# Optimization experiments

Hardware: AMD Instinct MI355X
Metric: run time of the kernel (lower is better)

The kernel has to match this reference:

```python
import jax, jax.numpy as jnp
import numpy as np

D_MODEL = 2048
N_HEADS = 16
N_KV = 4
HEAD_DIM = D_MODEL // N_HEADS  # 128
KV_DIM = N_KV * HEAD_DIM       # 512
CLIP = 8.0
EPS = 1e-5
THETA = 500000.0


def setup_inputs() -> dict:
    key = jax.random.key(0)
    ks = jax.random.split(key, 12)
    B, T = 2, 2048
    std = 0.02
    return {
        "x": jax.random.normal(ks[0], (B, T, D_MODEL), jnp.float32),
        "wq": jax.random.normal(ks[1], (D_MODEL, D_MODEL), jnp.float32) * std,
        "bq": jnp.zeros((D_MODEL,), jnp.float32),
        "wk": jax.random.normal(ks[2], (KV_DIM, D_MODEL), jnp.float32) * std,
        "bk": jnp.zeros((KV_DIM,), jnp.float32),
        "wv": jax.random.normal(ks[3], (KV_DIM, D_MODEL), jnp.float32) * std,
        "bv": jnp.zeros((KV_DIM,), jnp.float32),
        "wo": jax.random.normal(ks[4], (D_MODEL, D_MODEL), jnp.float32) * std,
        "bo": jnp.zeros((D_MODEL,), jnp.float32),
        "q_gamma": jnp.ones((D_MODEL,), jnp.float32),
        "q_beta": jnp.zeros((D_MODEL,), jnp.float32),
        "k_gamma": jnp.ones((KV_DIM,), jnp.float32),
        "k_beta": jnp.zeros((KV_DIM,), jnp.float32),
    }


def _layernorm(x, gamma, beta):
    mu = jnp.mean(x, axis=-1, keepdims=True)
    var = jnp.mean(jnp.square(x - mu), axis=-1, keepdims=True)
    return (x - mu) * jax.lax.rsqrt(var + EPS) * gamma + beta


def _rope(q, k):
    # q: (B,T,H,Dh), k: (B,T,Hkv,Dh); non-interleaved rotate-half RoPE
    T = q.shape[1]
    half = HEAD_DIM // 2
    inv_freq = 1.0 / (THETA ** (jnp.arange(0, half, dtype=jnp.float32) * 2.0 / HEAD_DIM))
    freqs = jnp.arange(T, dtype=jnp.float32)[:, None] * inv_freq[None, :]  # (T, half)
    emb = jnp.concatenate([freqs, freqs], axis=-1)  # (T, Dh)
    cos = jnp.cos(emb)[None, :, None, :]
    sin = jnp.sin(emb)[None, :, None, :]

    def rot_half(x):
        x1, x2 = x[..., :half], x[..., half:]
        return jnp.concatenate([-x2, x1], axis=-1)

    q = q * cos + rot_half(q) * sin
    k = k * cos + rot_half(k) * sin
    return q, k


def reference(x, wq, bq, wk, bk, wv, bv, wo, bo, q_gamma, q_beta, k_gamma, k_beta):
    B, T, _ = x.shape
    q = x @ wq.T + bq            # (B,T,D)
    k = x @ wk.T + bk            # (B,T,KV_DIM)
    v = x @ wv.T + bv
    q = jnp.clip(q, -CLIP, CLIP)
    k = jnp.clip(k, -CLIP, CLIP)
    v = jnp.clip(v, -CLIP, CLIP)
    q = _layernorm(q, q_gamma, q_beta)
    k = _layernorm(k, k_gamma, k_beta)
    q = q.reshape(B, T, N_HEADS, HEAD_DIM)
    k = k.reshape(B, T, N_KV, HEAD_DIM)
    v = v.reshape(B, T, N_KV, HEAD_DIM)
    q, k = _rope(q, k)
    # to (B,H,T,Dh)
    q = q.transpose(0, 2, 1, 3)
    k = k.transpose(0, 2, 1, 3)
    v = v.transpose(0, 2, 1, 3)
    g = N_HEADS // N_KV
    # GQA repeat_interleave via broadcast: (B,Hkv,T,Dh) -> (B,H,T,Dh)
    k = jnp.broadcast_to(k[:, :, None], (B, N_KV, g, T, HEAD_DIM)).reshape(B, N_HEADS, T, HEAD_DIM)
    v = jnp.broadcast_to(v[:, :, None], (B, N_KV, g, T, HEAD_DIM)).reshape(B, N_HEADS, T, HEAD_DIM)
    scale = 1.0 / jnp.sqrt(jnp.float32(HEAD_DIM))
    scores = jnp.einsum('bhqd,bhkd->bhqk', q, k) * scale
    causal = jnp.tril(jnp.ones((T, T), dtype=bool))
    scores = jnp.where(causal[None, None], scores, jnp.finfo(scores.dtype).min)
    att = jax.nn.softmax(scores, axis=-1)
    out = jnp.einsum('bhqk,bhkd->bhqd', att, v)     # (B,H,T,Dh)
    out = out.transpose(0, 2, 1, 3).reshape(B, T, D_MODEL)
    return out @ wo.T + bo
```

## Files before the change

### kernel.cpp

```cpp
#include <hip/hip_runtime.h>
#include <hip/hip_bf16.h>
#include <math.h>

typedef __bf16 bf16;
typedef __attribute__((ext_vector_type(8))) bf16 bf16x8;
typedef __attribute__((ext_vector_type(2))) bf16 bf16x2;
typedef __attribute__((ext_vector_type(4))) float f32x4;

#define LOG2E 1.4426950408889634f
#define LOG2_THETA 18.931568569324174f

#if __has_builtin(__builtin_amdgcn_exp2f)
#define EXP2F __builtin_amdgcn_exp2f
#else
#define EXP2F exp2f
#endif

__device__ inline void async_cp16(const void* gptr, void* lptr) {
  __builtin_amdgcn_global_load_lds(
      (const __attribute__((address_space(1))) unsigned int*)gptr,
      (__attribute__((address_space(3))) unsigned int*)lptr, 16, 0, 0);
}

__global__ __launch_bounds__(256) void cast_all(
    const float* __restrict__ x,  const float* __restrict__ wq,
    const float* __restrict__ wk, const float* __restrict__ wv,
    const float* __restrict__ wo, bf16* __restrict__ xb,
    bf16* __restrict__ wqkvb, bf16* __restrict__ wob) {
  const int bx = blockIdx.x;
  const size_t gi = ((size_t)bx * 256 + threadIdx.x) * 8;
  const float* src;
  bf16* dst;
  if (bx < 4096)      { src = x  + gi;              dst = xb + gi; }
  else if (bx < 6144) { src = wq + (gi -  8388608); dst = wqkvb + (gi - 8388608); }
  else if (bx < 6656) { src = wk + (gi - 12582912); dst = wqkvb + 4194304 + (gi - 12582912); }
  else if (bx < 7168) { src = wv + (gi - 13631488); dst = wqkvb + 5242880 + (gi - 13631488); }
  else                { src = wo + (gi - 14680064); dst = wob + (gi - 14680064); }
  float4 a = *(const float4*)(src);
  float4 b = *(const float4*)(src + 4);
  bf16x8 o;
  o[0] = (bf16)a.x; o[1] = (bf16)a.y; o[2] = (bf16)a.z; o[3] = (bf16)a.w;
  o[4] = (bf16)b.x; o[5] = (bf16)b.y; o[6] = (bf16)b.z; o[7] = (bf16)b.w;
  *(bf16x8*)dst = o;
}

template <typename OUT_T, bool QKV, bool CLIP>
__global__ __launch_bounds__(256) void gemm_bt(
    const bf16* __restrict__ A, const bf16* __restrict__ W,
    const float* __restrict__ b0, const float* __restrict__ b1,
    const float* __restrict__ b2, OUT_T* __restrict__ C,
    int M, int N, int K) {
  __shared__ bf16 As[2][128 * 32];
  __shared__ bf16 Bs[2][128 * 32];
  const int nwg = gridDim.x * gridDim.y;
  int lid = blockIdx.x + gridDim.x * blockIdx.y;
  lid = (lid & 7) * (nwg >> 3) + (lid >> 3);
  const int m0 = (lid & 31) * 128, n0 = (lid >> 5) * 128;
  const int t = threadIdx.x;
  const int w = t >> 6, lane = t & 63, quad = lane >> 4, l15 = lane & 15;
  const int wm = (w >> 1) * 64, wn = (w & 1) * 64;

  f32x4 acc[4][4];
#pragma unroll
  for (int i = 0; i < 4; i++)
#pragma unroll
    for (int j = 0; j < 4; j++) acc[i][j] = (f32x4)0.0f;

  int soff[2], ldso[2];
#pragma unroll
  for (int i = 0; i < 2; i++) {
    const int c = w * 128 + i * 64 + lane;
    const int r = c >> 2;
    const int sl = (c & 3) ^ (r & 3);
    soff[i] = r * K + sl * 8;
    ldso[i] = (w * 128 + i * 64) * 16;
  }
  const bf16* Abase = A + (size_t)m0 * K;
  const bf16* Wbase = W + (size_t)n0 * K;

  const int fseg = (quad ^ (l15 & 3)) * 8;

#pragma unroll
  for (int i = 0; i < 2; i++) {
    async_cp16(Abase + soff[i], (char*)&As[0][0] + ldso[i]);
    async_cp16(Wbase + soff[i], (char*)&Bs[0][0] + ldso[i]);
  }
  __asm__ volatile("s_waitcnt vmcnt(0)" ::: "memory");
  __builtin_amdgcn_s_barrier();
  __builtin_amdgcn_sched_barrier(0);

  int cur = 0;
  for (int k0 = 0; k0 < K; k0 += 32) {
    if (k0 + 32 < K) {
      const int nxt = cur ^ 1;
#pragma unroll
      for (int i = 0; i < 2; i++) {
        async_cp16(Abase + k0 + 32 + soff[i], (char*)&As[nxt][0] + ldso[i]);
        async_cp16(Wbase + k0 + 32 + soff[i], (char*)&Bs[nxt][0] + ldso[i]);
      }
    }
    __builtin_amdgcn_sched_barrier(0);

    bf16x8 af[4], bfr[4];
#pragma unroll
    for (int i = 0; i < 4; i++)
      af[i] = *(const bf16x8*)(&As[cur][0] + (wm + i * 16 + l15) * 32 + fseg);
#pragma unroll
    for (int j = 0; j < 4; j++)
      bfr[j] = *(const bf16x8*)(&Bs[cur][0] + (wn + j * 16 + l15) * 32 + fseg);
#pragma unroll
    for (int i = 0; i < 4; i++)
#pragma unroll
      for (int j = 0; j < 4; j++)
        acc[i][j] = __builtin_amdgcn_mfma_f32_16x16x32_bf16(af[i], bfr[j], acc[i][j], 0, 0, 0);

    __asm__ volatile("s_waitcnt vmcnt(0)" ::: "memory");
    __builtin_amdgcn_s_barrier();
    __builtin_amdgcn_sched_barrier(0);
    cur ^= 1;
  }

#pragma unroll
  for (int i = 0; i < 4; i++)
#pragma unroll
    for (int j = 0; j < 4; j++) {
      const int col = n0 + wn + j * 16 + l15;
      float bval;
      if (QKV) {
        if (col < 2048) bval = b0[col];
        else if (col < 2560) bval = b1[col - 2048];
        else bval = b2[col - 2560];
      } else {
        bval = b0[col];
      }
#pragma unroll
      for (int r = 0; r < 4; r++) {
        const int row = m0 + wm + i * 16 + quad * 4 + r;
        float v = acc[i][j][r] + bval;
        if (CLIP) v = fminf(fmaxf(v, -8.0f), 8.0f);
        C[(size_t)row * N + col] = (OUT_T)v;
      }
    }
}

__global__ __launch_bounds__(256) void fused_mid(
    const bf16* __restrict__ X, const float* __restrict__ qg,
    const float* __restrict__ qb, const float* __restrict__ kg,
    const float* __restrict__ kb, bf16* __restrict__ Qr,
    bf16* __restrict__ Kr, bf16* __restrict__ Vt) {
  __shared__ bf16 smt[64][136];
  __shared__ float red[8];
  __shared__ float tcs[64], tsn[64];
  __shared__ float ktab_c[4][64], ktab_s[4][64];
  const int bx = blockIdx.x;
  const int tid = threadIdx.x;
  const int w = tid >> 6, lane = tid & 63;

  if (bx < 4096) {
    const int row = bx, b = row >> 11, tpos = row & 2047;
    if (tid < 64) {
      const float inv = exp2f((float)tid * (-LOG2_THETA / 64.0f));
      float sn, cs;
      sincosf((float)tpos * inv, &sn, &cs);
      tcs[tid] = cs; tsn[tid] = sn;
    }
    const bf16* x = X + (size_t)row * 3072;
    bf16x8 xi = *(const bf16x8*)(x + tid * 8);
    float v[8];
    float s = 0.0f;
#pragma unroll
    for (int e = 0; e < 8; e++) { v[e] = (float)xi[e]; s += v[e]; }
#pragma unroll
    for (int m = 32; m >= 1; m >>= 1) s += __shfl_xor(s, m, 64);
    if (lane == 0) red[w] = s;
    __syncthreads();
    const float mean = (red[0] + red[1] + red[2] + red[3]) * (1.0f / 2048.0f);
    float vs = 0.0f;
#pragma unroll
    for (int e = 0; e < 8; e++) { float d = v[e] - mean; vs += d * d; }
#pragma unroll
    for (int m = 32; m >= 1; m >>= 1) vs += __shfl_xor(vs, m, 64);
    if (lane == 0) red[4 + w] = vs;
    __syncthreads();
    const float var = (red[4] + red[5] + red[6] + red[7]) * (1.0f / 2048.0f);
    const float rstd = rsqrtf(var + 1e-5f);
    const int c0 = tid * 8;
    const float4 g0 = *(const float4*)(qg + c0);
    const float4 g1 = *(const float4*)(qg + c0 + 4);
    const float4 b0v = *(const float4*)(qb + c0);
    const float4 b1v = *(const float4*)(qb + c0 + 4);
    const float gA[8] = {g0.x, g0.y, g0.z, g0.w, g1.x, g1.y, g1.z, g1.w};
    const float bA[8] = {b0v.x, b0v.y, b0v.z, b0v.w, b1v.x, b1v.y, b1v.z, b1v.w};
    float y[8];
#pragma unroll
    for (int e = 0; e < 8; e++) y[e] = (v[e] - mean) * rstd * gA[e] + bA[e];
    const int h = c0 >> 7;
    bf16x8 ov;
#pragma unroll
    for (int e = 0; e < 8; e++) {
      const int c = c0 + e, d = c & 127, i = d & 63;
      const float part = __shfl_xor(y[e], 8, 64);
      const float rot = (d < 64) ? -part : part;
      ov[e] = (bf16)(y[e] * tcs[i] + rot * tsn[i]);
    }
    *(bf16x8*)(Qr + ((size_t)(b * 16 + h) * 2048 + tpos) * 128 + (c0 & 127)) = ov;
  } else if (bx < 5120) {
    const int idx = bx - 4096;
    const int row = idx * 4 + w, b = row >> 11, tpos = row & 2047;
    {
      const float inv = exp2f((float)lane * (-LOG2_THETA / 64.0f));
      float sn, cs;
      sincosf((float)tpos * inv, &sn, &cs);
      ktab_c[w][lane] = cs; ktab_s[w][lane] = sn;
    }
    __syncthreads();
    const bf16* x = X + (size_t)row * 3072 + 2048;
    bf16x8 xi = *(const bf16x8*)(x + lane * 8);
    float v[8];
    float s = 0.0f;
#pragma unroll
    for (int e = 0; e < 8; e++) { v[e] = (float)xi[e]; s += v[e]; }
#pragma unroll
    for (int m = 32; m >= 1; m >>= 1) s += __shfl_xor(s, m, 64);
    const float mean = s * (1.0f / 512.0f);
    float vs = 0.0f;
#pragma unroll
    for (int e = 0; e < 8; e++) { float d = v[e] - mean; vs += d * d; }
#pragma unroll
    for (int m = 32; m >= 1; m >>= 1) vs += __shfl_xor(vs, m, 64);
    const float var = vs * (1.0f / 512.0f);
    const float rstd = rsqrtf(var + 1e-5f);
    const int c0 = lane * 8;
    const float4 g0 = *(const float4*)(kg + c0);
    const float4 g1 = *(const float4*)(kg + c0 + 4);
    const float4 b0v = *(const float4*)(kb + c0);
    const float4 b1v = *(const float4*)(kb + c0 + 4);
    const float gA[8] = {g0.x, g0.y, g0.z, g0.w, g1.x, g1.y, g1.z, g1.w};
    const float bA[8] = {b0v.x, b0v.y, b0v.z, b0v.w, b1v.x, b1v.y, b1v.z, b1v.w};
    float y[8];
#pragma unroll
    for (int e = 0; e < 8; e++) y[e] = (v[e] - mean) * rstd * gA[e] + bA[e];
    const int kv = c0 >> 7;
    bf16x8 ov;
#pragma unroll
    for (int e = 0; e < 8; e++) {
      const int c = c0 + e, d = c & 127, i = d & 63;
      const float part = __shfl_xor(y[e], 8, 64);
      const float rot = (d < 64) ? -part : part;
      ov[e] = (bf16)(y[e] * ktab_c[w][i] + rot * ktab_s[w][i]);
    }
    *(bf16x8*)(Kr + ((size_t)(b * 4 + kv) * 2048 + tpos) * 128 + (c0 & 127)) = ov;
  } else {
    const int idx = bx - 5120;
    const int b = idx >> 7, kv = (idx >> 5) & 3, t0 = (idx & 31) * 64;
#pragma unroll
    for (int i = 0; i < 4; i++) {
      const int c = i * 256 + tid;
      const int r = c >> 4, d8 = (c & 15) * 8;
      *(bf16x8*)&smt[r][d8] =
          *(const bf16x8*)(X + (size_t)(b * 2048 + t0 + r) * 3072 + 2560 + kv * 128 + d8);
    }
    __syncthreads();
#pragma unroll
    for (int i = 0; i < 4; i++) {
      const int c = i * 256 + tid;
      const int d = c >> 3, t8 = (c & 7) * 8;
      bf16x8 o;
#pragma unroll
      for (int j = 0; j < 8; j++) o[j] = smt[t8 + j][d];
      *(bf16x8*)(Vt + (size_t)((b * 4 + kv) * 128 + d) * 2048 + t0 + t8) = o;
    }
  }
}

__global__ __launch_bounds__(256) void flash_attn(
    const bf16* __restrict__ Q, const bf16* __restrict__ Kt,
    const bf16* __restrict__ Vt, bf16* __restrict__ O) {
  const int p = blockIdx.x;
  const int h = blockIdx.y, b = blockIdx.z;
  const int kv = h >> 2;
  const int tid = threadIdx.x;
  const int w = tid >> 6, lane = tid & 63, quad = lane >> 4, l15 = lane & 15;

  __shared__ bf16 Ks[64][128];
  __shared__ bf16 Vs[128][64];
  __shared__ bf16 Ps[4][16][88];

  const bf16* Kb = Kt + (size_t)(b * 4 + kv) * 2048 * 128;
  const bf16* Vb = Vt + (size_t)(b * 4 + kv) * 128 * 2048;

  const int ksl = lane & 15, krt = lane >> 4;
  const int vsl = lane & 7,  vdt = lane >> 3;
  int kgo[4], vgo[4];
  bf16 *kwp[4], *vwp[4];
#pragma unroll
  for (int i = 0; i < 4; i++) {
    const int c = w * 4 + i;
    const int rt = c * 4 + krt;
    kgo[i] = rt * 128 + ksl * 8;
    kwp[i] = &Ks[rt][(ksl ^ (rt & 15)) * 8];
    const int d = c * 8 + vdt;
    vgo[i] = d * 2048 + vsl * 8;
    vwp[i] = &Vs[d][(vsl ^ (d & 7)) * 8];
  }

  const float cexp = 0.08838834764831845f * LOG2E;
  bf16x8 ones;
#pragma unroll
  for (int i = 0; i < 8; i++) ones[i] = (bf16)1.0f;

#pragma unroll 1
  for (int pass = 0; pass < 2; pass++) {
    const int qb = (pass == 0) ? (31 - p) : p;
    const int q0 = qb * 64;
    const int nkt = qb + 1;

    const bf16* Qb = Q + ((size_t)(b * 16 + h) * 2048 + q0 + w * 16 + l15) * 128;
    bf16x8 aq[4];
#pragma unroll
    for (int kk = 0; kk < 4; kk++) aq[kk] = *(const bf16x8*)(Qb + kk * 32 + quad * 8);

    f32x4 o[9];
#pragma unroll
    for (int dt = 0; dt < 9; dt++) o[dt] = (f32x4)0.0f;

    bf16x8 kreg[4], vreg[4];
#pragma unroll
    for (int i = 0; i < 4; i++) {
      kreg[i] = *(const bf16x8*)(Kb + kgo[i]);
      vreg[i] = *(const bf16x8*)(Vb + vgo[i]);
    }

#pragma unroll 1
    for (int kt = 0; kt < nkt; kt++) {
      const int k0 = kt * 64;
      __syncthreads();
#pragma unroll
      for (int i = 0; i < 4; i++) {
        *(bf16x8*)kwp[i] = kreg[i];
        *(bf16x8*)vwp[i] = vreg[i];
      }
      __syncthreads();

      if (kt + 1 < nkt) {
        const size_t kb2 = (size_t)(k0 + 64);
#pragma unroll
        for (int i = 0; i < 4; i++) {
          kreg[i] = *(const bf16x8*)(Kb + kb2 * 128 + kgo[i]);
          vreg[i] = *(const bf16x8*)(Vb + kb2 + vgo[i]);
        }
      }

      f32x4 s4[4];
#pragma unroll
      for (int j = 0; j < 4; j++) {
        f32x4 acc = (f32x4)0.0f;
        const int n = j * 16 + l15;
#pragma unroll
        for (int kk = 0; kk < 4; kk++) {
          bf16x8 bk = *(const bf16x8*)(
              &Ks[0][0] + n * 128 + (((kk * 4 + quad) ^ l15) * 8));
          acc = __builtin_amdgcn_mfma_f32_16x16x32_bf16(aq[kk], bk, acc, 0, 0, 0);
        }
        s4[j] = acc;
      }

      const bool diag = (kt == qb);
      const int qrow_base = q0 + w * 16 + quad * 4;
#pragma unroll
      for (int j = 0; j < 4; j++) {
        const int kg = k0 + j * 16 + l15;
#pragma unroll
        for (int r = 0; r < 4; r++) {
          float pv = EXP2F(s4[j][r] * cexp);
          if (diag && kg > qrow_base + r) pv = 0.0f;
          Ps[w][quad * 4 + r][j * 16 + l15] = (bf16)pv;
        }
      }
      __asm__ volatile("s_waitcnt lgkmcnt(0)" ::: "memory");

#pragma unroll
      for (int kk = 0; kk < 2; kk++) {
        bf16x8 pa = *(const bf16x8*)&Ps[w][l15][kk * 32 + quad * 8];
#pragma unroll
        for (int dt = 0; dt < 8; dt++) {
          const int d = dt * 16 + l15;
          bf16x8 vb = *(const bf16x8*)(
              &Vs[0][0] + d * 64 + (((kk * 4 + quad) ^ (d & 7)) * 8));
          o[dt] = __builtin_amdgcn_mfma_f32_16x16x32_bf16(pa, vb, o[dt], 0, 0, 0);
        }
        o[8] = __builtin_amdgcn_mfma_f32_16x16x32_bf16(pa, ones, o[8], 0, 0, 0);
      }
    }

    bf16* Ob = O + ((size_t)(b * 2048 + q0 + w * 16 + quad * 4)) * 2048 + h * 128;
#pragma unroll
    for (int r = 0; r < 4; r++) {
      const float rinv = 1.0f / o[8][r];
#pragma unroll
      for (int dt = 0; dt < 8; dt++)
        Ob[(size_t)r * 2048 + dt * 16 + l15] = (bf16)(o[dt][r] * rinv);
    }
  }
}

extern "C" void kernel_launch(void* const* d_in, const int* in_sizes, int n_in,
                              void* d_out, int out_size, void* d_ws, size_t ws_size,
                              hipStream_t stream) {
  const float* x   = (const float*)d_in[0];
  const float* wq  = (const float*)d_in[1];
  const float* bq  = (const float*)d_in[2];
  const float* wk  = (const float*)d_in[3];
  const float* bk  = (const float*)d_in[4];
  const float* wv  = (const float*)d_in[5];
  const float* bv  = (const float*)d_in[6];
  const float* wo  = (const float*)d_in[7];
  const float* bo  = (const float*)d_in[8];
  const float* qg  = (const float*)d_in[9];
  const float* qbt = (const float*)d_in[10];
  const float* kg  = (const float*)d_in[11];
  const float* kbt = (const float*)d_in[12];
  float* out = (float*)d_out;

  char* ws = (char*)d_ws;
  if (ws_size < (size_t)88080384) return;
  bf16* xb    = (bf16*)(ws);
  bf16* wqkvb = (bf16*)(ws + 16777216);
  bf16* wob   = (bf16*)(ws + 29360128);
  bf16* qkvb  = (bf16*)(ws + 37748736);
  bf16* Qr    = (bf16*)(ws + 62914560);
  bf16* Kr    = (bf16*)(ws + 79691776);
  bf16* Vt    = (bf16*)(ws + 83886080);
  bf16* At    = (bf16*)(ws);

  cast_all<<<9216, 256, 0, stream>>>(x, wq, wk, wv, wo, xb, wqkvb, wob);
  gemm_bt<bf16, true, true><<<dim3(32, 24), 256, 0, stream>>>(
      xb, wqkvb, bq, bk, bv, qkvb, 4096, 3072, 2048);
  fused_mid<<<5376, 256, 0, stream>>>(qkvb, qg, qbt, kg, kbt, Qr, Kr, Vt);
  flash_attn<<<dim3(16, 16, 2), 256, 0, stream>>>(Qr, Kr, Vt, At);
  gemm_bt<float, false, false><<<dim3(32, 16), 256, 0, stream>>>(
      At, wob, bo, nullptr, nullptr, out, 4096, 2048, 2048);
}
```

Before: 311.9 us.

## Double-buffer K/V tiles in LDS with one barrier per iteration

```diff
diff --git a/kernel.cpp b/kernel.cpp
--- a/kernel.cpp
+++ b/kernel.cpp
@@ -282,8 +282,8 @@
   const int tid = threadIdx.x;
   const int w = tid >> 6, lane = tid & 63, quad = lane >> 4, l15 = lane & 15;
 
-  __shared__ bf16 Ks[64][128];
-  __shared__ bf16 Vs[128][64];
+  __shared__ bf16 Ks[2][64][128];
+  __shared__ bf16 Vs[2][128][64];
   __shared__ bf16 Ps[4][16][88];
 
   const bf16* Kb = Kt + (size_t)(b * 4 + kv) * 2048 * 128;
@@ -291,17 +291,16 @@
 
   const int ksl = lane & 15, krt = lane >> 4;
   const int vsl = lane & 7,  vdt = lane >> 3;
-  int kgo[4], vgo[4];
-  bf16 *kwp[4], *vwp[4];
+  int kgo[4], vgo[4], kwo[4], vwo[4];
 #pragma unroll
   for (int i = 0; i < 4; i++) {
     const int c = w * 4 + i;
     const int rt = c * 4 + krt;
     kgo[i] = rt * 128 + ksl * 8;
-    kwp[i] = &Ks[rt][(ksl ^ (rt & 15)) * 8];
+    kwo[i] = rt * 128 + ((ksl ^ (rt & 15)) * 8);
     const int d = c * 8 + vdt;
     vgo[i] = d * 2048 + vsl * 8;
-    vwp[i] = &Vs[d][(vsl ^ (d & 7)) * 8];
+    vwo[i] = d * 64 + ((vsl ^ (d & 7)) * 8);
   }
 
   const float cexp = 0.08838834764831845f * LOG2E;
@@ -330,40 +329,60 @@
       kreg[i] = *(const bf16x8*)(Kb + kgo[i]);
       vreg[i] = *(const bf16x8*)(Vb + vgo[i]);
     }
+#pragma unroll
+    for (int i = 0; i < 4; i++) {
+      *(bf16x8*)(&Ks[0][0][0] + kwo[i]) = kreg[i];
+      *(bf16x8*)(&Vs[0][0][0] + vwo[i]) = vreg[i];
+    }
+    if (nkt > 1) {
+#pragma unroll
+      for (int i = 0; i < 4; i++) {
+        kreg[i] = *(const bf16x8*)(Kb + (size_t)64 * 128 + kgo[i]);
+        vreg[i] = *(const bf16x8*)(Vb + 64 + vgo[i]);
+      }
+    }
+    __asm__ volatile("s_waitcnt lgkmcnt(0)" ::: "memory");
+    __builtin_amdgcn_s_barrier();
+    __builtin_amdgcn_sched_barrier(0);
 
 #pragma unroll 1
     for (int kt = 0; kt < nkt; kt++) {
+      const int cur = kt & 1;
       const int k0 = kt * 64;
-      __syncthreads();
-#pragma unroll
-      for (int i = 0; i < 4; i++) {
-        *(bf16x8*)kwp[i] = kreg[i];
-        *(bf16x8*)vwp[i] = vreg[i];
-      }
-      __syncthreads();
 
       if (kt + 1 < nkt) {
-        const size_t kb2 = (size_t)(k0 + 64);
+        const int nb = cur ^ 1;
+        bf16* kdst = &Ks[nb][0][0];
+        bf16* vdst = &Vs[nb][0][0];
 #pragma unroll
         for (int i = 0; i < 4; i++) {
-          kreg[i] = *(const bf16x8*)(Kb + kb2 * 128 + kgo[i]);
-          vreg[i] = *(const bf16x8*)(Vb + kb2 + vgo[i]);
+          *(bf16x8*)(kdst + kwo[i]) = kreg[i];
+          *(bf16x8*)(vdst + vwo[i]) = vreg[i];
         }
       }
-
+      if (kt + 2 < nkt) {
+#pragma unroll
+        for (int i = 0; i < 4; i++) {
+          kreg[i] = *(const bf16x8*)(Kb + (size_t)(k0 + 128) * 128 + kgo[i]);
+          vreg[i] = *(const bf16x8*)(Vb + (size_t)(k0 + 128) + vgo[i]);
+        }
+      }
+
+      const bf16* ksrc = &Ks[cur][0][0];
       f32x4 s4[4];
+      __builtin_amdgcn_s_setprio(1);
 #pragma unroll
       for (int j = 0; j < 4; j++) {
         f32x4 acc = (f32x4)0.0f;
         const int n = j * 16 + l15;
 #pragma unroll
         for (int kk = 0; kk < 4; kk++) {
-          bf16x8 bk = *(const bf16x8*)(
-              &Ks[0][0] + n * 128 + (((kk * 4 + quad) ^ l15) * 8));
+          bf16x8 bk = *(const bf16x8*)(ksrc + n * 128 + (((kk * 4 + quad) ^ l15) * 8));
           acc = __builtin_amdgcn_mfma_f32_16x16x32_bf16(aq[kk], bk, acc, 0, 0, 0);
         }
         s4[j] = acc;
       }
+      __builtin_amdgcn_s_setprio(0);
 
       const bool diag = (kt == qb);
       const int qrow_base = q0 + w * 16 + quad * 4;
@@ -379,18 +398,24 @@
       }
       __asm__ volatile("s_waitcnt lgkmcnt(0)" ::: "memory");
 
+      const bf16* vsrc = &Vs[cur][0][0];
+      __builtin_amdgcn_s_setprio(1);
 #pragma unroll
       for (int kk = 0; kk < 2; kk++) {
         bf16x8 pa = *(const bf16x8*)&Ps[w][l15][kk * 32 + quad * 8];
 #pragma unroll
         for (int dt = 0; dt < 8; dt++) {
           const int d = dt * 16 + l15;
-          bf16x8 vb = *(const bf16x8*)(
-              &Vs[0][0] + d * 64 + (((kk * 4 + quad) ^ (d & 7)) * 8));
+          bf16x8 vb = *(const bf16x8*)(vsrc + d * 64 + (((kk * 4 + quad) ^ (d & 7)) * 8));
           o[dt] = __builtin_amdgcn_mfma_f32_16x16x32_bf16(pa, vb, o[dt], 0, 0, 0);
         }
         o[8] = __builtin_amdgcn_mfma_f32_16x16x32_bf16(pa, ones, o[8], 0, 0, 0);
       }
+      __builtin_amdgcn_s_setprio(0);
+
+      __asm__ volatile("s_waitcnt lgkmcnt(0)" ::: "memory");
+      __builtin_amdgcn_s_barrier();
+      __builtin_amdgcn_sched_barrier(0);
     }
 
     bf16* Ob = O + ((size_t)(b * 2048 + q0 + w * 16 + quad * 4)) * 2048 + h * 128;
```

After: 316.6 us. Within noise of the previous version (+1.5%).

## Process paired causal query blocks in one pass sharing K/V tiles

Applied to the files above, without the earlier changes.

```diff
diff --git a/kernel.cpp b/kernel.cpp
--- a/kernel.cpp
+++ b/kernel.cpp
@@ -309,48 +309,51 @@
 #pragma unroll
   for (int i = 0; i < 8; i++) ones[i] = (bf16)1.0f;
 
+  const int qbA = 31 - p, qbB = p;
+  const int q0A = qbA * 64, q0B = qbB * 64;
+  const int nkt = qbA + 1;
+
+  const bf16* QbA = Q + ((size_t)(b * 16 + h) * 2048 + q0A + w * 16 + l15) * 128;
+  const bf16* QbB = Q + ((size_t)(b * 16 + h) * 2048 + q0B + w * 16 + l15) * 128;
+  bf16x8 aqA[4], aqB[4];
+#pragma unroll
+  for (int kk = 0; kk < 4; kk++) {
+    aqA[kk] = *(const bf16x8*)(QbA + kk * 32 + quad * 8);
+    aqB[kk] = *(const bf16x8*)(QbB + kk * 32 + quad * 8);
+  }
+
+  f32x4 oA[9], oB[9];
+#pragma unroll
+  for (int dt = 0; dt < 9; dt++) { oA[dt] = (f32x4)0.0f; oB[dt] = (f32x4)0.0f; }
+
+  bf16x8 kreg[4], vreg[4];
+#pragma unroll
+  for (int i = 0; i < 4; i++) {
+    kreg[i] = *(const bf16x8*)(Kb + kgo[i]);
+    vreg[i] = *(const bf16x8*)(Vb + vgo[i]);
+  }
+
 #pragma unroll 1
-  for (int pass = 0; pass < 2; pass++) {
-    const int qb = (pass == 0) ? (31 - p) : p;
-    const int q0 = qb * 64;
-    const int nkt = qb + 1;
-
-    const bf16* Qb = Q + ((size_t)(b * 16 + h) * 2048 + q0 + w * 16 + l15) * 128;
-    bf16x8 aq[4];
-#pragma unroll
-    for (int kk = 0; kk < 4; kk++) aq[kk] = *(const bf16x8*)(Qb + kk * 32 + quad * 8);
-
-    f32x4 o[9];
-#pragma unroll
-    for (int dt = 0; dt < 9; dt++) o[dt] = (f32x4)0.0f;
-
-    bf16x8 kreg[4], vreg[4];
+  for (int kt = 0; kt < nkt; kt++) {
+    const int k0 = kt * 64;
+    __syncthreads();
 #pragma unroll
     for (int i = 0; i < 4; i++) {
-      kreg[i] = *(const bf16x8*)(Kb + kgo[i]);
-      vreg[i] = *(const bf16x8*)(Vb + vgo[i]);
-    }
-
-#pragma unroll 1
-    for (int kt = 0; kt < nkt; kt++) {
-      const int k0 = kt * 64;
-      __syncthreads();
+      *(bf16x8*)kwp[i] = kreg[i];
+      *(bf16x8*)vwp[i] = vreg[i];
+    }
+    __syncthreads();
+
+    if (kt + 1 < nkt) {
+      const size_t kb2 = (size_t)(k0 + 64);
 #pragma unroll
       for (int i = 0; i < 4; i++) {
-        *(bf16x8*)kwp[i] = kreg[i];
-        *(bf16x8*)vwp[i] = vreg[i];
-      }
-      __syncthreads();
-
-      if (kt + 1 < nkt) {
-        const size_t kb2 = (size_t)(k0 + 64);
-#pragma unroll
-        for (int i = 0; i < 4; i++) {
-          kreg[i] = *(const bf16x8*)(Kb + kb2 * 128 + kgo[i]);
-          vreg[i] = *(const bf16x8*)(Vb + kb2 + vgo[i]);
-        }
-      }
-
+        kreg[i] = *(const bf16x8*)(Kb + kb2 * 128 + kgo[i]);
+        vreg[i] = *(const bf16x8*)(Vb + kb2 + vgo[i]);
+      }
+    }
+
+    {
       f32x4 s4[4];
 #pragma unroll
       for (int j = 0; j < 4; j++) {
@@ -360,13 +363,12 @@
         for (int kk = 0; kk < 4; kk++) {
           bf16x8 bk = *(const bf16x8*)(
               &Ks[0][0] + n * 128 + (((kk * 4 + quad) ^ l15) * 8));
-          acc = __builtin_amdgcn_mfma_f32_16x16x32_bf16(aq[kk], bk, acc, 0, 0, 0);
+          acc = __builtin_amdgcn_mfma_f32_16x16x32_bf16(aqA[kk], bk, acc, 0, 0, 0);
         }
         s4[j] = acc;
       }
-
-      const bool diag = (kt == qb);
-      const int qrow_base = q0 + w * 16 + quad * 4;
+      const bool diag = (kt == qbA);
+      const int qrow_base = q0A + w * 16 + quad * 4;
 #pragma unroll
       for (int j = 0; j < 4; j++) {
         const int kg = k0 + j * 16 + l15;
@@ -378,7 +380,6 @@
         }
       }
       __asm__ volatile("s_waitcnt lgkmcnt(0)" ::: "memory");
-
 #pragma unroll
       for (int kk = 0; kk < 2; kk++) {
         bf16x8 pa = *(const bf16x8*)&Ps[w][l15][kk * 32 + quad * 8];
@@ -387,19 +388,72 @@
           const int d = dt * 16 + l15;
           bf16x8 vb = *(const bf16x8*)(
               &Vs[0][0] + d * 64 + (((kk * 4 + quad) ^ (d & 7)) * 8));
-          o[dt] = __builtin_amdgcn_mfma_f32_16x16x32_bf16(pa, vb, o[dt], 0, 0, 0);
-        }
-        o[8] = __builtin_amdgcn_mfma_f32_16x16x32_bf16(pa, ones, o[8], 0, 0, 0);
-      }
-    }
-
-    bf16* Ob = O + ((size_t)(b * 2048 + q0 + w * 16 + quad * 4)) * 2048 + h * 128;
+          oA[dt] = __builtin_amdgcn_mfma_f32_16x16x32_bf16(pa, vb, oA[dt], 0, 0, 0);
+        }
+        oA[8] = __builtin_amdgcn_mfma_f32_16x16x32_bf16(pa, ones, oA[8], 0, 0, 0);
+      }
+    }
+
+    if (kt <= qbB) {
+      f32x4 s4[4];
+#pragma unroll
+      for (int j = 0; j < 4; j++) {
+        f32x4 acc = (f32x4)0.0f;
+        const int n = j * 16 + l15;
+#pragma unroll
+        for (int kk = 0; kk < 4; kk++) {
+          bf16x8 bk = *(const bf16x8*)(
+              &Ks[0][0] + n * 128 + (((kk * 4 + quad) ^ l15) * 8));
+          acc = __builtin_amdgcn_mfma_f32_16x16x32_bf16(aqB[kk], bk, acc, 0, 0, 0);
+        }
+        s4[j] = acc;
+      }
+      const bool diag = (kt == qbB);
+      const int qrow_base = q0B + w * 16 + quad * 4;
+#pragma unroll
+      for (int j = 0; j < 4; j++) {
+        const int kg = k0 + j * 16 + l15;
+#pragma unroll
+        for (int r = 0; r < 4; r++) {
+          float pv = EXP2F(s4[j][r] * cexp);
+          if (diag && kg > qrow_base + r) pv = 0.0f;
+          Ps[w][quad * 4 + r][j * 16 + l15] = (bf16)pv;
+        }
+      }
+      __asm__ volatile("s_waitcnt lgkmcnt(0)" ::: "memory");
+#pragma unroll
+      for (int kk = 0; kk < 2; kk++) {
+        bf16x8 pa = *(const bf16x8*)&Ps[w][l15][kk * 32 + quad * 8];
+#pragma unroll
+        for (int dt = 0; dt < 8; dt++) {
+          const int d = dt * 16 + l15;
+          bf16x8 vb = *(const bf16x8*)(
+              &Vs[0][0] + d * 64 + (((kk * 4 + quad) ^ (d & 7)) * 8));
+          oB[dt] = __builtin_amdgcn_mfma_f32_16x16x32_bf16(pa, vb, oB[dt], 0, 0, 0);
+        }
+        oB[8] = __builtin_amdgcn_mfma_f32_16x16x32_bf16(pa, ones, oB[8], 0, 0, 0);
+      }
+    }
+  }
+
+  {
+    bf16* Ob = O + ((size_t)(b * 2048 + q0A + w * 16 + quad * 4)) * 2048 + h * 128;
 #pragma unroll
     for (int r = 0; r < 4; r++) {
-      const float rinv = 1.0f / o[8][r];
+      const float rinv = 1.0f / oA[8][r];
 #pragma unroll
       for (int dt = 0; dt < 8; dt++)
-        Ob[(size_t)r * 2048 + dt * 16 + l15] = (bf16)(o[dt][r] * rinv);
+        Ob[(size_t)r * 2048 + dt * 16 + l15] = (bf16)(oA[dt][r] * rinv);
+    }
+  }
+  {
+    bf16* Ob = O + ((size_t)(b * 2048 + q0B + w * 16 + quad * 4)) * 2048 + h * 128;
+#pragma unroll
+    for (int r = 0; r < 4; r++) {
+      const float rinv = 1.0f / oB[8][r];
+#pragma unroll
+      for (int dt = 0; dt < 8; dt++)
+        Ob[(size_t)r * 2048 + dt * 16 + l15] = (bf16)(oB[dt][r] * rinv);
     }
   }
 }
```

Result: no change. 311.7 us (-0.0%).
